# Optimization experiments

Hardware: AMD Instinct MI355X
Metric: run time of the kernel (lower is better)

Reference implementation:

```python
import jax, jax.numpy as jnp
import numpy as np

B, N, C = 128, 197, 768
H = 12
HID = 3072
DROP = 0.1
EPS = 1e-5


def _layernorm(x, g, b):
    m = jnp.mean(x, axis=-1, keepdims=True)
    v = jnp.var(x, axis=-1, keepdims=True)
    return (x - m) * jax.lax.rsqrt(v + EPS) * g + b


def setup_inputs() -> dict:
    key = jax.random.key(0)
    ks = jax.random.split(key, 6)
    def lin(k, fan_in, fan_out):
        return (jax.random.normal(k, (fan_in, fan_out), jnp.float32) * (fan_in ** -0.5))
    return {
        "x": jax.random.normal(ks[0], (B, N, C), jnp.float32),
        "ln1_g": jnp.ones((C,), jnp.float32),
        "ln1_b": jnp.zeros((C,), jnp.float32),
        "Wqkv": lin(ks[1], C, 3 * C),          # qkv_bias=False
        "Wproj": lin(ks[2], C, C),
        "bproj": jnp.zeros((C,), jnp.float32),
        "ln2_g": jnp.ones((C,), jnp.float32),
        "ln2_b": jnp.zeros((C,), jnp.float32),
        "W1": lin(ks[3], C, HID),
        "b1": jnp.zeros((HID,), jnp.float32),
        "W2": lin(ks[4], HID, C),
        "b2": jnp.zeros((C,), jnp.float32),
    }


def reference(x, ln1_g, ln1_b, Wqkv, Wproj, bproj, ln2_g, ln2_b, W1, b1, W2, b2):
    Bx, Nx, Cx = x.shape
    hd = Cx // H
    thr = int((Nx - 1) * DROP)            # 19
    keep = (Nx - 1) - (thr + 1)           # 176 patches kept (rank > thr)

    # ---- drop_low_attn: unscaled q@k^T, mean over heads, cls->patch scores ----
    qkv = (x @ Wqkv).reshape(Bx, Nx, 3, H, hd).transpose(2, 0, 3, 1, 4)
    q, k = qkv[0], qkv[1]
    attn0 = jnp.einsum('bhnd,bhmd->bhnm', q, k)        # no scale, no softmax
    scores = jnp.mean(attn0, axis=1)[:, 0, 1:]          # [B, N-1]
    rank = jnp.argsort(jnp.argsort(scores, axis=1), axis=1)
    keep_mask = rank > thr                              # exactly `keep` True per row
    # indices of kept patches in original order (stable argsort of ~mask)
    idx = jnp.argsort((~keep_mask).astype(jnp.int32), axis=1)[:, :keep] + 1
    tok = jnp.concatenate([jnp.zeros((Bx, 1), idx.dtype), idx], axis=1)  # cls + kept
    x = jnp.take_along_axis(x, tok[:, :, None], axis=1) / (1.0 - DROP)   # [B, 177, C]
    Np = keep + 1

    # ---- attention block (scaled softmax attention) ----
    h = _layernorm(x, ln1_g, ln1_b)
    qkv2 = (h @ Wqkv).reshape(Bx, Np, 3, H, hd).transpose(2, 0, 3, 1, 4)
    q2, k2, v2 = qkv2[0], qkv2[1], qkv2[2]
    a = jax.nn.softmax(jnp.einsum('bhnd,bhmd->bhnm', q2, k2) * (hd ** -0.5), axis=-1)
    o = jnp.einsum('bhnm,bhmd->bhnd', a, v2).transpose(0, 2, 1, 3).reshape(Bx, Np, Cx)
    x = x + (o @ Wproj + bproj)

    # ---- MLP block ----
    h = _layernorm(x, ln2_g, ln2_b)
    x = x + (jax.nn.gelu(h @ W1 + b1, approximate=False) @ W2 + b2)
    return x
```

## Files before the change

### kernel.cpp

```cpp
#include <hip/hip_runtime.h>
#include <math.h>

#define BB 128
#define NTOK 197
#define CC 768
#define HH 12
#define HD 64
#define HIDN 3072
#define NP 177
#define NPATCH 196
#define THRK 19
#define MR (BB*NP)

using short8 = __attribute__((ext_vector_type(8))) short;
using f32x4  = __attribute__((ext_vector_type(4))) float;

__device__ __forceinline__ unsigned short f2b(float f){
  unsigned u = __builtin_bit_cast(unsigned, f);
  u += 0x7fffu + ((u >> 16) & 1u);
  return (unsigned short)(u >> 16);
}

__device__ __forceinline__ float fast_gelu(float v){
  float u = v * 0.70710678118654752f;
  float a = fabsf(u);
  float t = 1.0f / fmaf(0.3275911f, a, 1.0f);
  float p = fmaf(1.061405429f, t, -1.453152027f);
  p = fmaf(p, t, 1.421413741f);
  p = fmaf(p, t, -0.284496736f);
  p = fmaf(p, t, 0.254829592f);
  p = p * t;
  float e = __expf(-a*a);
  float erfu = copysignf(1.0f - p*e, u);
  return 0.5f * v * (1.0f + erfu);
}

__device__ __forceinline__ void gload16(const void* src, void* lds){
  __builtin_amdgcn_global_load_lds(
      (const __attribute__((address_space(1))) unsigned int*)src,
      (__attribute__((address_space(3))) unsigned int*)lds,
      16, 0, 0);
}

__global__ void tcvt_kernel(const float* __restrict__ in, unsigned short* __restrict__ out, int K, int N){
  __shared__ float tile[64][65];
  int n0 = blockIdx.x*64, k0 = blockIdx.y*64;
  int t = threadIdx.x;
  int r = t >> 6, c = t & 63;
  #pragma unroll
  for (int i = 0; i < 16; ++i)
    tile[r + i*4][c] = in[(size_t)(k0 + r + i*4)*N + n0 + c];
  __syncthreads();
  #pragma unroll
  for (int i = 0; i < 16; ++i)
    out[(size_t)(n0 + r + i*4)*K + k0 + c] = f2b(tile[c][r + i*4]);
}

__global__ void q0_kernel(const float* __restrict__ x, const float* __restrict__ Wqkv, float* __restrict__ q0){
  int b = blockIdx.x, t = threadIdx.x;
  int c = blockIdx.y*256 + t;
  __shared__ float xs[CC];
  for (int j = t; j < CC; j += 256) xs[j] = x[(size_t)b*NTOK*CC + j];
  __syncthreads();
  double acc = 0.0;
  for (int j = 0; j < CC; ++j) acc = fma((double)xs[j], (double)Wqkv[(size_t)j*(3*CC) + c], acc);
  q0[b*CC + c] = (float)acc;
}

__global__ void wvec_kernel(const float* __restrict__ Wqkv, const float* __restrict__ q0, float* __restrict__ wv){
  int b = blockIdx.x;
  int j = blockIdx.y*4 + (threadIdx.x >> 6);
  int l = threadIdx.x & 63;
  const float* row = Wqkv + (size_t)j*(3*CC) + CC;
  const float* qs = q0 + b*CC;
  double acc = 0.0;
  for (int c = l; c < CC; c += 64) acc = fma((double)row[c], (double)qs[c], acc);
  for (int off = 32; off; off >>= 1) acc += __shfl_down(acc, off);
  if (l == 0) wv[b*CC + j] = (float)acc;
}

__global__ void score_kernel(const float* __restrict__ x, const float* __restrict__ wv, float* __restrict__ sc){
  int m = blockIdx.x, b = blockIdx.y, l = threadIdx.x;
  const float* xr = x + ((size_t)b*NTOK + 1 + m)*CC;
  const float* wr = wv + b*CC;
  double acc = 0.0;
  for (int c = l; c < CC; c += 64) acc = fma((double)xr[c], (double)wr[c], acc);
  for (int off = 32; off; off >>= 1) acc += __shfl_down(acc, off);
  if (l == 0) sc[b*NPATCH + m] = (float)(acc * (1.0/12.0));
}

__global__ void select_kernel(const float* __restrict__ sc, int* __restrict__ tok){
  int b = blockIdx.x, t = threadIdx.x;
  __shared__ float s[NPATCH];
  __shared__ int kp[NPATCH];
  for (int m = t; m < NPATCH; m += 256) s[m] = sc[b*NPATCH + m];
  __syncthreads();
  for (int m = t; m < NPATCH; m += 256){
    float v = s[m]; int rank = 0;
    for (int j = 0; j < NPATCH; ++j){
      float u = s[j];
      rank += (u < v) || (u == v && j < m);
    }
    kp[m] = (rank > THRK) ? 1 : 0;
  }
  __syncthreads();
  for (int m = t; m < NPATCH; m += 256){
    if (kp[m]){
      int pos = 0;
      for (int j = 0; j < m; ++j) pos += kp[j];
      tok[b*NP + 1 + pos] = m + 1;
    }
  }
  if (t == 0) tok[b*NP] = 0;
}

__global__ void gather_kernel(const float* __restrict__ x, const int* __restrict__ tok, float* __restrict__ xk){
  int i = blockIdx.x, b = blockIdx.y, t = threadIdx.x;
  int src = tok[b*NP + i];
  const float* xr = x + ((size_t)b*NTOK + src)*CC;
  float* o = xk + ((size_t)b*NP + i)*CC;
  for (int c = t; c < CC; c += 256) o[c] = xr[c] * (1.0f/0.9f);
}

__global__ void ln_kernel(const float* __restrict__ in, const float* __restrict__ g,
                          const float* __restrict__ bt, unsigned short* __restrict__ out){
  int row = blockIdx.x, t = threadIdx.x;
  const float* xr = in + (size_t)row*CC;
  float v0 = xr[t], v1 = xr[t+256], v2 = xr[t+512];
  float s = v0+v1+v2, ss = v0*v0+v1*v1+v2*v2;
  for (int off = 32; off; off >>= 1){ s += __shfl_down(s, off); ss += __shfl_down(ss, off); }
  __shared__ float red[8];
  int wid = t >> 6, lane = t & 63;
  if (lane == 0){ red[wid] = s; red[4+wid] = ss; }
  __syncthreads();
  if (t == 0){
    float S = red[0]+red[1]+red[2]+red[3], SS = red[4]+red[5]+red[6]+red[7];
    float mean = S * (1.0f/CC);
    float var = SS * (1.0f/CC) - mean*mean;
    red[0] = mean; red[1] = rsqrtf(var + 1e-5f);
  }
  __syncthreads();
  float mean = red[0], rstd = red[1];
  unsigned short* orow = out + (size_t)row*CC;
  orow[t]     = f2b((v0-mean)*rstd*g[t]     + bt[t]);
  orow[t+256] = f2b((v1-mean)*rstd*g[t+256] + bt[t+256]);
  orow[t+512] = f2b((v2-mean)*rstd*g[t+512] + bt[t+512]);
}

template<int EPI>
__global__ __launch_bounds__(256, 3) void gemm128(
    const unsigned short* __restrict__ A, const unsigned short* __restrict__ Bt,
    const float* __restrict__ bias, const float* __restrict__ res, void* __restrict__ outp,
    int M, int N, int K)
{
  __shared__ __align__(16) short lds[3*8192];
  int nwg = gridDim.x, o = blockIdx.x;
  int q = nwg >> 3, rr = nwg & 7;
  int xcd = o & 7, seq = o >> 3;
  int wg = (xcd < rr) ? xcd*(q+1) + seq : rr*(q+1) + (xcd - rr)*q + seq;
  int nx = N >> 7;
  int m0 = (wg / nx) << 7, n0 = (wg % nx) << 7;

  int t = threadIdx.x, w = t >> 6, l = t & 63;
  int wr = w >> 1, wc = w & 1;
  f32x4 acc[4][4] = {};
  int nt = K >> 5;

  auto stage = [&](int kti, int sb){
    int kt = kti << 5;
    short* buf = &lds[sb*8192];
    #pragma unroll
    for (int j = 0; j < 2; ++j){
      int row = j*64 + w*16 + (l >> 2);
      int gk = ((l & 3) ^ ((row >> 1) & 3)) * 8;
      gload16(A  + (size_t)(m0 + row)*K + kt + gk, &buf[(j*64 + w*16)*32]);
      gload16(Bt + (size_t)(n0 + row)*K + kt + gk, &buf[4096 + (j*64 + w*16)*32]);
    }
  };
  auto compute = [&](int cb){
    const short* Ab = &lds[cb*8192];
    const short* Bb = Ab + 4096;
    short8 af[4], bf[4];
    #pragma unroll
    for (int i = 0; i < 4; ++i){
      int Ra = wr*64 + i*16 + (l & 15);
      af[i] = *reinterpret_cast<const short8*>(&Ab[Ra*32 + (((l>>4) ^ ((Ra>>1)&3)))*8]);
      int Rb = wc*64 + i*16 + (l & 15);
      bf[i] = *reinterpret_cast<const short8*>(&Bb[Rb*32 + (((l>>4) ^ ((Rb>>1)&3)))*8]);
    }
    __builtin_amdgcn_s_setprio(1);
    #pragma unroll
    for (int i = 0; i < 4; ++i)
      #pragma unroll
      for (int jn = 0; jn < 4; ++jn)
        acc[i][jn] = __builtin_amdgcn_mfma_f32_16x16x32_bf16(af[i], bf[jn], acc[i][jn], 0, 0, 0);
    __builtin_amdgcn_s_setprio(0);
  };
  auto step = [&](int ti, int cb, int sb){
    bool more = (ti + 2) < nt;
    if (more) stage(ti + 2, sb);
    compute(cb);
    if (more) asm volatile("s_waitcnt vmcnt(4)" ::: "memory");
    else      asm volatile("s_waitcnt vmcnt(0)" ::: "memory");
    __builtin_amdgcn_s_barrier();
    asm volatile("" ::: "memory");
  };

  stage(0, 0); stage(1, 1);
  asm volatile("s_waitcnt vmcnt(4)" ::: "memory");
  __builtin_amdgcn_s_barrier();
  asm volatile("" ::: "memory");

  #pragma unroll 1
  for (int ti = 0; ti < nt; ti += 3){
    step(ti,     0, 2);
    step(ti + 1, 1, 0);
    step(ti + 2, 2, 1);
  }

  #pragma unroll
  for (int i = 0; i < 4; ++i)
  #pragma unroll
  for (int jn = 0; jn < 4; ++jn){
    int row = m0 + wr*64 + i*16 + (l>>4)*4;
    int col = n0 + wc*64 + jn*16 + (l&15);
    #pragma unroll
    for (int r = 0; r < 4; ++r){
      float v = acc[i][jn][r];
      if (EPI != 0) v += bias[col];
      if (EPI == 2) v = fast_gelu(v);
      if (EPI == 1 || EPI == 3) v += res[(size_t)(row+r)*N + col];
      if (EPI == 0 || EPI == 2) ((unsigned short*)outp)[(size_t)(row+r)*N + col] = f2b(v);
      else                      ((float*)outp)[(size_t)(row+r)*N + col] = v;
    }
  }
}

__global__ __launch_bounds__(256) void attn_kernel(const unsigned short* __restrict__ qkv2,
                                                   unsigned short* __restrict__ o)
{
  int rt = blockIdx.x, h = blockIdx.y, b = blockIdx.z;
  int t = threadIdx.x, w = t >> 6, l = t & 63;
  __shared__ short Vt[64*192];
  __shared__ short P[4][16*192];
  for (int idx = t; idx < NP*8; idx += 256){
    int m = idx >> 3, d0 = (idx & 7)*8;
    short8 v = *reinterpret_cast<const short8*>(qkv2 + (size_t)(b*NP+m)*(3*CC) + 2*CC + h*HD + d0);
    #pragma unroll
    for (int j = 0; j < 8; ++j) Vt[(d0+j)*192 + m] = v[j];
  }
  for (int idx = t; idx < 64*15; idx += 256){
    int d = idx/15, m = NP + idx%15;
    Vt[d*192 + m] = 0;
  }
  __syncthreads();
  int nb = rt*64 + w*16;
  int g = l >> 4, c = l & 15;
  int nq = nb + c; if (nq > NP-1) nq = NP-1;
  const unsigned short* qrow = qkv2 + (size_t)(b*NP+nq)*(3*CC) + h*HD + 8*g;
  short8 aq0 = *reinterpret_cast<const short8*>(qrow);
  short8 aq1 = *reinterpret_cast<const short8*>(qrow + 32);
  f32x4 acc[12];
  #pragma unroll
  for (int ct = 0; ct < 12; ++ct){
    int m = ct*16 + c; if (m > NP-1) m = NP-1;
    const unsigned short* krow = qkv2 + (size_t)(b*NP+m)*(3*CC) + CC + h*HD + 8*g;
    short8 bk0 = *reinterpret_cast<const short8*>(krow);
    short8 bk1 = *reinterpret_cast<const short8*>(krow + 32);
    f32x4 a = {};
    a = __builtin_amdgcn_mfma_f32_16x16x32_bf16(aq0, bk0, a, 0, 0, 0);
    a = __builtin_amdgcn_mfma_f32_16x16x32_bf16(aq1, bk1, a, 0, 0, 0);
    acc[ct] = a;
  }
  float mx[4] = {-INFINITY, -INFINITY, -INFINITY, -INFINITY};
  #pragma unroll
  for (int ct = 0; ct < 12; ++ct){
    bool valid = (ct*16 + c) < NP;
    #pragma unroll
    for (int r = 0; r < 4; ++r){
      float v = valid ? acc[ct][r]*0.125f : -INFINITY;
      acc[ct][r] = v;
      mx[r] = fmaxf(mx[r], v);
    }
  }
  #pragma unroll
  for (int off = 1; off < 16; off <<= 1){
    #pragma unroll
    for (int r = 0; r < 4; ++r) mx[r] = fmaxf(mx[r], __shfl_xor(mx[r], off));
  }
  float sm2[4] = {0.f, 0.f, 0.f, 0.f};
  #pragma unroll
  for (int ct = 0; ct < 12; ++ct)
    #pragma unroll
    for (int r = 0; r < 4; ++r){
      float e = __expf(acc[ct][r] - mx[r]);
      acc[ct][r] = e; sm2[r] += e;
    }
  #pragma unroll
  for (int off = 1; off < 16; off <<= 1){
    #pragma unroll
    for (int r = 0; r < 4; ++r) sm2[r] += __shfl_xor(sm2[r], off);
  }
  float inv[4];
  #pragma unroll
  for (int r = 0; r < 4; ++r) inv[r] = 1.0f / sm2[r];
  #pragma unroll
  for (int ct = 0; ct < 12; ++ct)
    #pragma unroll
    for (int r = 0; r < 4; ++r)
      P[w][(4*g + r)*192 + ct*16 + c] = (short)f2b(acc[ct][r]*inv[r]);
  f32x4 acc2[4] = {};
  __builtin_amdgcn_s_setprio(1);
  #pragma unroll
  for (int ks = 0; ks < 6; ++ks){
    short8 pa = *reinterpret_cast<const short8*>(&P[w][c*192 + ks*32 + 8*g]);
    #pragma unroll
    for (int ct2 = 0; ct2 < 4; ++ct2){
      short8 bv = *reinterpret_cast<const short8*>(&Vt[(ct2*16 + c)*192 + ks*32 + 8*g]);
      acc2[ct2] = __builtin_amdgcn_mfma_f32_16x16x32_bf16(pa, bv, acc2[ct2], 0, 0, 0);
    }
  }
  __builtin_amdgcn_s_setprio(0);
  #pragma unroll
  for (int ct2 = 0; ct2 < 4; ++ct2){
    #pragma unroll
    for (int r = 0; r < 4; ++r){
      int n = nb + 4*g + r;
      if (n < NP) o[(size_t)(b*NP+n)*CC + h*HD + ct2*16 + c] = f2b(acc2[ct2][r]);
    }
  }
}

extern "C" void kernel_launch(void* const* d_in, const int* in_sizes, int n_in,
                              void* d_out, int out_size, void* d_ws, size_t ws_size,
                              hipStream_t stream) {
  const float* x     = (const float*)d_in[0];
  const float* ln1g  = (const float*)d_in[1];
  const float* ln1b  = (const float*)d_in[2];
  const float* Wqkv  = (const float*)d_in[3];
  const float* Wproj = (const float*)d_in[4];
  const float* bproj = (const float*)d_in[5];
  const float* ln2g  = (const float*)d_in[6];
  const float* ln2b  = (const float*)d_in[7];
  const float* W1    = (const float*)d_in[8];
  const float* b1    = (const float*)d_in[9];
  const float* W2    = (const float*)d_in[10];
  const float* b2    = (const float*)d_in[11];
  float* out = (float*)d_out;

  unsigned char* base = (unsigned char*)d_ws;
  size_t off = 0;
  auto alloc = [&](size_t bytes) -> void* {
    off = (off + 255) & ~(size_t)255;
    void* p = base + off;
    off += bytes;
    return p;
  };
  unsigned short* WqkvT  = (unsigned short*)alloc((size_t)(3*CC)*CC*2);
  unsigned short* WprojT = (unsigned short*)alloc((size_t)CC*CC*2);
  unsigned short* W1T    = (unsigned short*)alloc((size_t)HIDN*CC*2);
  unsigned short* W2T    = (unsigned short*)alloc((size_t)CC*HIDN*2);
  float* q0   = (float*)alloc((size_t)BB*CC*4);
  float* wv   = (float*)alloc((size_t)BB*CC*4);
  float* sc   = (float*)alloc((size_t)BB*NPATCH*4);
  int*   tok  = (int*)alloc((size_t)BB*NP*4);
  unsigned short* hbuf = (unsigned short*)alloc((size_t)MR*CC*2);
  float* xk   = (float*)alloc((size_t)MR*CC*4);
  unsigned short* qkv2 = (unsigned short*)alloc((size_t)MR*3*CC*2);
  if (off > ws_size) return;

  unsigned short* obuf = hbuf;
  unsigned short* mid  = (unsigned short*)xk;
  float* x2 = out;

  tcvt_kernel<<<dim3((3*CC)/64, CC/64), 256, 0, stream>>>(Wqkv,  WqkvT,  CC, 3*CC);
  tcvt_kernel<<<dim3(CC/64, CC/64),     256, 0, stream>>>(Wproj, WprojT, CC, CC);
  tcvt_kernel<<<dim3(HIDN/64, CC/64),   256, 0, stream>>>(W1,    W1T,    CC, HIDN);
  tcvt_kernel<<<dim3(CC/64, HIDN/64),   256, 0, stream>>>(W2,    W2T,    HIDN, CC);

  q0_kernel<<<dim3(BB, 3), 256, 0, stream>>>(x, Wqkv, q0);
  wvec_kernel<<<dim3(BB, CC/4), 256, 0, stream>>>(Wqkv, q0, wv);
  score_kernel<<<dim3(NPATCH, BB), 64, 0, stream>>>(x, wv, sc);
  select_kernel<<<BB, 256, 0, stream>>>(sc, tok);
  gather_kernel<<<dim3(NP, BB), 256, 0, stream>>>(x, tok, xk);

  ln_kernel<<<MR, 256, 0, stream>>>(xk, ln1g, ln1b, hbuf);
  gemm128<0><<<(MR/128)*((3*CC)/128), 256, 0, stream>>>(hbuf, WqkvT, nullptr, nullptr, qkv2, MR, 3*CC, CC);
  attn_kernel<<<dim3(3, HH, BB), 256, 0, stream>>>(qkv2, obuf);
  gemm128<1><<<(MR/128)*(CC/128), 256, 0, stream>>>(obuf, WprojT, bproj, xk, x2, MR, CC, CC);

  ln_kernel<<<MR, 256, 0, stream>>>(x2, ln2g, ln2b, hbuf);
  gemm128<2><<<(MR/128)*(HIDN/128), 256, 0, stream>>>(hbuf, W1T, b1, nullptr, mid, MR, HIDN, CC);
  gemm128<3><<<(MR/128)*(CC/128), 256, 0, stream>>>(mid, W2T, b2, x2, out, MR, CC, HIDN);
}
```

Before: 767.2 us.

## Deepen GEMM LDS pipeline to five stages with register double-buffered fragments

The bf16 MFMA GEMM now keeps five LDS stages with four tiles of global loads in flight instead of two, and double-buffers the A/B fragment registers so the LDS reads for the next k-tile overlap the current MFMAs. The aim is to hide global memory and LDS read latency behind matrix math. In exchange LDS use rises from 48 KB to 80 KB and the occupancy hint drops from 3 to 2 workgroups per CU, which reduces the latency hiding that comes from concurrency. The wait-count logic is also more complex, and buffer reuse could race if the counts are wrong.

```diff
diff --git a/kernel.cpp b/kernel.cpp
--- a/kernel.cpp
+++ b/kernel.cpp
@@ -148,12 +148,12 @@
 }
 
 template<int EPI>
-__global__ __launch_bounds__(256, 3) void gemm128(
+__global__ __launch_bounds__(256, 2) void gemm128(
     const unsigned short* __restrict__ A, const unsigned short* __restrict__ Bt,
     const float* __restrict__ bias, const float* __restrict__ res, void* __restrict__ outp,
     int M, int N, int K)
 {
-  __shared__ __align__(16) short lds[3*8192];
+  __shared__ __align__(16) short lds[5*8192];
   int nwg = gridDim.x, o = blockIdx.x;
   int q = nwg >> 3, rr = nwg & 7;
   int xcd = o & 7, seq = o >> 3;
@@ -166,9 +166,9 @@
   f32x4 acc[4][4] = {};
   int nt = K >> 5;
 
-  auto stage = [&](int kti, int sb){
+  auto stage = [&](int kti){
     int kt = kti << 5;
-    short* buf = &lds[sb*8192];
+    short* buf = &lds[(kti % 5)*8192];
     #pragma unroll
     for (int j = 0; j < 2; ++j){
       int row = j*64 + w*16 + (l >> 2);
@@ -177,10 +177,9 @@
       gload16(Bt + (size_t)(n0 + row)*K + kt + gk, &buf[4096 + (j*64 + w*16)*32]);
     }
   };
-  auto compute = [&](int cb){
-    const short* Ab = &lds[cb*8192];
+  auto readf = [&](int kti, short8* af, short8* bf){
+    const short* Ab = &lds[(kti % 5)*8192];
     const short* Bb = Ab + 4096;
-    short8 af[4], bf[4];
     #pragma unroll
     for (int i = 0; i < 4; ++i){
       int Ra = wr*64 + i*16 + (l & 15);
@@ -188,6 +187,8 @@
       int Rb = wc*64 + i*16 + (l & 15);
       bf[i] = *reinterpret_cast<const short8*>(&Bb[Rb*32 + (((l>>4) ^ ((Rb>>1)&3)))*8]);
     }
+  };
+  auto mfma16 = [&](short8* af, short8* bf){
     __builtin_amdgcn_s_setprio(1);
     #pragma unroll
     for (int i = 0; i < 4; ++i)
@@ -196,26 +197,37 @@
         acc[i][jn] = __builtin_amdgcn_mfma_f32_16x16x32_bf16(af[i], bf[jn], acc[i][jn], 0, 0, 0);
     __builtin_amdgcn_s_setprio(0);
   };
-  auto step = [&](int ti, int cb, int sb){
-    bool more = (ti + 2) < nt;
-    if (more) stage(ti + 2, sb);
-    compute(cb);
-    if (more) asm volatile("s_waitcnt vmcnt(4)" ::: "memory");
-    else      asm volatile("s_waitcnt vmcnt(0)" ::: "memory");
+  auto endwait = [&](int p){
+    if (p + 4 < nt)      asm volatile("s_waitcnt vmcnt(8)" ::: "memory");
+    else if (p + 3 < nt) asm volatile("s_waitcnt vmcnt(4)" ::: "memory");
+    else if (p + 2 < nt) asm volatile("s_waitcnt vmcnt(0)" ::: "memory");
     __builtin_amdgcn_s_barrier();
     asm volatile("" ::: "memory");
   };
 
-  stage(0, 0); stage(1, 1);
-  asm volatile("s_waitcnt vmcnt(4)" ::: "memory");
+  short8 afA[4], bfA[4], afB[4], bfB[4];
+
+  stage(0); stage(1); stage(2); stage(3);
+  asm volatile("s_waitcnt vmcnt(8)" ::: "memory");
   __builtin_amdgcn_s_barrier();
   asm volatile("" ::: "memory");
+  readf(0, afA, bfA);
 
   #pragma unroll 1
-  for (int ti = 0; ti < nt; ti += 3){
-    step(ti,     0, 2);
-    step(ti + 1, 1, 0);
-    step(ti + 2, 2, 1);
+  for (int ti = 0; ti < nt; ti += 2){
+    {
+      if (ti + 4 < nt) stage(ti + 4);
+      readf(ti + 1, afB, bfB);
+      mfma16(afA, bfA);
+      endwait(ti);
+    }
+    {
+      int u = ti + 1;
+      if (u + 4 < nt) stage(u + 4);
+      if (u + 1 < nt) readf(u + 1, afA, bfA);
+      mfma16(afB, bfB);
+      if (u + 1 < nt) endwait(u);
+    }
   }
 
   #pragma unroll
```

New measurement: 806.7 us. 1.05x slower.
